# Kernel tuning notes

Hardware: AMD Instinct MI355X
Metric: run time of the kernel (lower is better)

Reference implementation:

```python
import jax, jax.numpy as jnp
import numpy as np

NUM_CLASSES = 100
EPS = 1e-07


def setup_inputs() -> dict:
    key = jax.random.key(0)
    k1, k2 = jax.random.split(key)
    N = 1_000_000
    logits = jax.random.normal(k1, (N, NUM_CLASSES), dtype=jnp.float32)
    labels = jax.random.randint(k2, (N,), 0, NUM_CLASSES, dtype=jnp.int32)
    return {"logits": logits, "labels": labels}


def reference(logits, labels):
    # pred: [N] argmax class per sample
    pred = jnp.argmax(logits, axis=1)
    C = NUM_CLASSES
    zeros = jnp.zeros((C,), dtype=jnp.float32)
    # single-pass confusion-matrix marginals (replaces per-class python loop)
    pred_count = zeros.at[pred].add(1.0)          # tp_c + fp_c
    true_count = zeros.at[labels].add(1.0)        # tp_c + fn_c
    correct = (pred == labels).astype(jnp.float32)
    tp = zeros.at[labels].add(correct)            # tp_c
    fp = pred_count - tp
    fn = true_count - tp
    precision = tp / (tp + fp + EPS)
    recall = tp / (tp + fn + EPS)
    # beta = 1 -> (1 + 1) * p * r / (1 * p + r + eps)
    f1 = 2.0 * precision * recall / (precision + recall + EPS)
    return jnp.mean(f1)
```

## Files before the change

### kernel.cpp

```cpp
#include <hip/hip_runtime.h>

#define NCLS 100
#define EPS 1e-7f

__global__ void zero_counts_kernel(unsigned int* __restrict__ counts) {
    int i = threadIdx.x;
    if (i < 3 * NCLS) counts[i] = 0u;
}

__global__ __launch_bounds__(256) void hist_kernel(
        const float* __restrict__ logits,
        const int* __restrict__ labels,
        unsigned int* __restrict__ counts,
        int N) {
    __shared__ unsigned int s_pred[NCLS];
    __shared__ unsigned int s_true[NCLS];
    __shared__ unsigned int s_tp[NCLS];
    for (int i = threadIdx.x; i < NCLS; i += blockDim.x) {
        s_pred[i] = 0u; s_true[i] = 0u; s_tp[i] = 0u;
    }
    __syncthreads();

    const int tid    = blockIdx.x * blockDim.x + threadIdx.x;
    const int q      = tid & 3;
    const int quad   = tid >> 2;
    const int nquads = (gridDim.x * blockDim.x) >> 2;

    const float4* f4base = (const float4*)logits;

    for (int row = quad; row < N; row += nquads) {
        const size_t rowf4 = (size_t)row * 25;
        const size_t A     = rowf4 & ~(size_t)3;
        const int    r3    = row & 3;

        float4 v[7];
        #pragma unroll
        for (int k = 0; k < 7; ++k) v[k] = f4base[A + 4 * k + q];

        const int off = (q - r3) << 2;

        float best = -INFINITY;
        int bidx = 0;
        #pragma unroll
        for (int k = 0; k < 7; ++k) {
            const int cb = 16 * k + off;
            float4 w = v[k];
            if ((unsigned)(cb + 0) < (unsigned)NCLS && w.x > best) { best = w.x; bidx = cb;     }
            if ((unsigned)(cb + 1) < (unsigned)NCLS && w.y > best) { best = w.y; bidx = cb + 1; }
            if ((unsigned)(cb + 2) < (unsigned)NCLS && w.z > best) { best = w.z; bidx = cb + 2; }
            if ((unsigned)(cb + 3) < (unsigned)NCLS && w.w > best) { best = w.w; bidx = cb + 3; }
        }

        #pragma unroll
        for (int m = 1; m <= 2; m <<= 1) {
            float ob = __shfl_xor(best, m, 64);
            int   oi = __shfl_xor(bidx, m, 64);
            if (ob > best || (ob == best && oi < bidx)) { best = ob; bidx = oi; }
        }

        if (q == 0) {
            int lab = labels[row];
            atomicAdd(&s_pred[bidx], 1u);
            atomicAdd(&s_true[lab], 1u);
            if (bidx == lab) atomicAdd(&s_tp[lab], 1u);
        }
    }

    __syncthreads();
    for (int i = threadIdx.x; i < NCLS; i += blockDim.x) {
        unsigned int v;
        if ((v = s_pred[i]) != 0u) atomicAdd(&counts[i], v);
        if ((v = s_true[i]) != 0u) atomicAdd(&counts[NCLS + i], v);
        if ((v = s_tp[i])   != 0u) atomicAdd(&counts[2 * NCLS + i], v);
    }
}

__global__ void finalize_kernel(const unsigned int* __restrict__ counts,
                                float* __restrict__ out) {
    __shared__ float s_f1[NCLS];
    int c = threadIdx.x;
    if (c < NCLS) {
        float tp    = (float)counts[2 * NCLS + c];
        float predc = (float)counts[c];
        float truec = (float)counts[NCLS + c];
        float fp = predc - tp;
        float fn = truec - tp;
        float precision = tp / (tp + fp + EPS);
        float recall    = tp / (tp + fn + EPS);
        float f1 = 2.0f * precision * recall / (precision + recall + EPS);
        s_f1[c] = f1;
    }
    __syncthreads();
    if (c == 0) {
        float sum = 0.0f;
        for (int i = 0; i < NCLS; ++i) sum += s_f1[i];
        out[0] = sum / (float)NCLS;
    }
}

extern "C" void kernel_launch(void* const* d_in, const int* in_sizes, int n_in,
                              void* d_out, int out_size, void* d_ws, size_t ws_size,
                              hipStream_t stream) {
    const float* logits = (const float*)d_in[0];
    const int*   labels = (const int*)d_in[1];
    float* out = (float*)d_out;
    unsigned int* counts = (unsigned int*)d_ws;

    const int N = in_sizes[1];

    zero_counts_kernel<<<1, 320, 0, stream>>>(counts);

    const int block = 256;
    const int grid  = 2048;
    hist_kernel<<<grid, block, 0, stream>>>(logits, labels, counts, N);

    finalize_kernel<<<1, 128, 0, stream>>>(counts, out);
}
```

Measured before the change: 533.0 us.

## Assign contiguous row chunks per block and double-buffer row loads

Replaces the grid-stride loop over 2048 blocks with one block per contiguous 512-row chunk, launching about 1954 blocks. Each wave now register double-buffers its row loads, issuing the next row's float4 and label loads before running argmax on the current row. The intent is to hide memory latency and improve locality for this bandwidth-bound 400MB scan. The cost is more registers per thread and a per-block shared-histogram flush that now covers fewer rows.

```diff
diff --git a/kernel.cpp b/kernel.cpp
--- a/kernel.cpp
+++ b/kernel.cpp
@@ -2,10 +2,57 @@
 
 #define NCLS 100
 #define EPS 1e-7f
+#define ROWS_PER_BLOCK 512
+#define N_ITER (ROWS_PER_BLOCK / 64)
 
 __global__ void zero_counts_kernel(unsigned int* __restrict__ counts) {
     int i = threadIdx.x;
     if (i < 3 * NCLS) counts[i] = 0u;
+}
+
+__device__ __forceinline__ void load7(const float4* __restrict__ f4,
+                                      int r, int q, int rowEnd,
+                                      float4 v[7], int* lab,
+                                      const int* __restrict__ labels) {
+    if (r < rowEnd) {
+        const size_t A = ((size_t)r * 25) & ~(size_t)3;
+        #pragma unroll
+        for (int k = 0; k < 7; ++k) v[k] = f4[A + 4 * k + q];
+        if (q == 0) *lab = labels[r];
+    }
+}
+
+__device__ __forceinline__ void process7(const float4 v[7], int r, int q,
+                                         int rowEnd, int lab,
+                                         unsigned int* s_pred,
+                                         unsigned int* s_true,
+                                         unsigned int* s_tp) {
+    float best = -INFINITY;
+    int bidx = 0;
+    if (r < rowEnd) {
+        const int r3 = r & 3;
+        const int off = (q - r3) << 2;
+        #pragma unroll
+        for (int k = 0; k < 7; ++k) {
+            const int cb = 16 * k + off;
+            float4 w = v[k];
+            if ((unsigned)(cb + 0) < (unsigned)NCLS && w.x > best) { best = w.x; bidx = cb;     }
+            if ((unsigned)(cb + 1) < (unsigned)NCLS && w.y > best) { best = w.y; bidx = cb + 1; }
+            if ((unsigned)(cb + 2) < (unsigned)NCLS && w.z > best) { best = w.z; bidx = cb + 2; }
+            if ((unsigned)(cb + 3) < (unsigned)NCLS && w.w > best) { best = w.w; bidx = cb + 3; }
+        }
+    }
+    #pragma unroll
+    for (int m = 1; m <= 2; m <<= 1) {
+        float ob = __shfl_xor(best, m, 64);
+        int   oi = __shfl_xor(bidx, m, 64);
+        if (ob > best || (ob == best && oi < bidx)) { best = ob; bidx = oi; }
+    }
+    if (q == 0 && r < rowEnd) {
+        atomicAdd(&s_pred[bidx], 1u);
+        atomicAdd(&s_true[lab], 1u);
+        if (bidx == lab) atomicAdd(&s_tp[lab], 1u);
+    }
 }
 
 __global__ __launch_bounds__(256) void hist_kernel(
@@ -21,49 +68,36 @@
     }
     __syncthreads();
 
-    const int tid    = blockIdx.x * blockDim.x + threadIdx.x;
-    const int q      = tid & 3;
-    const int quad   = tid >> 2;
-    const int nquads = (gridDim.x * blockDim.x) >> 2;
+    const int lane = threadIdx.x & 63;
+    const int wv   = threadIdx.x >> 6;
+    const int q    = lane & 3;
+    const int g    = lane >> 2;
 
-    const float4* f4base = (const float4*)logits;
+    const int blockStart = blockIdx.x * ROWS_PER_BLOCK;
+    const int rowEnd     = min(blockStart + ROWS_PER_BLOCK, N);
 
-    for (int row = quad; row < N; row += nquads) {
-        const size_t rowf4 = (size_t)row * 25;
-        const size_t A     = rowf4 & ~(size_t)3;
-        const int    r3    = row & 3;
+    const float4* f4 = (const float4*)logits;
 
-        float4 v[7];
-        #pragma unroll
-        for (int k = 0; k < 7; ++k) v[k] = f4base[A + 4 * k + q];
+    int row = blockStart + wv * 16 + g;
 
-        const int off = (q - r3) << 2;
+    float4 va[7], vb[7];
+    int la = 0, lb = 0;
 
-        float best = -INFINITY;
-        int bidx = 0;
-        #pragma unroll
-        for (int k = 0; k < 7; ++k) {
-            const int cb = 16 * k + off;
-            float4 w = v[k];
-            if ((unsigned)(cb + 0) < (unsigned)NCLS && w.x > best) { best = w.x; bidx = cb;     }
-            if ((unsigned)(cb + 1) < (unsigned)NCLS && w.y > best) { best = w.y; bidx = cb + 1; }
-            if ((unsigned)(cb + 2) < (unsigned)NCLS && w.z > best) { best = w.z; bidx = cb + 2; }
-            if ((unsigned)(cb + 3) < (unsigned)NCLS && w.w > best) { best = w.w; bidx = cb + 3; }
+    load7(f4, row, q, rowEnd, va, &la, labels);
+
+    #pragma unroll 1
+    for (int i = 0; i < N_ITER; i += 2) {
+        const int r1 = row + 64;
+        load7(f4, r1, q, rowEnd, vb, &lb, labels);
+        process7(va, row, q, rowEnd, la, s_pred, s_true, s_tp);
+
+        const int r2 = r1 + 64;
+        if (i + 2 < N_ITER) {
+            load7(f4, r2, q, rowEnd, va, &la, labels);
         }
+        process7(vb, r1, q, rowEnd, lb, s_pred, s_true, s_tp);
 
-        #pragma unroll
-        for (int m = 1; m <= 2; m <<= 1) {
-            float ob = __shfl_xor(best, m, 64);
-            int   oi = __shfl_xor(bidx, m, 64);
-            if (ob > best || (ob == best && oi < bidx)) { best = ob; bidx = oi; }
-        }
-
-        if (q == 0) {
-            int lab = labels[row];
-            atomicAdd(&s_pred[bidx], 1u);
-            atomicAdd(&s_true[lab], 1u);
-            if (bidx == lab) atomicAdd(&s_tp[lab], 1u);
-        }
+        row = r2;
     }
 
     __syncthreads();
@@ -111,7 +145,7 @@
     zero_counts_kernel<<<1, 320, 0, stream>>>(counts);
 
     const int block = 256;
-    const int grid  = 2048;
+    const int grid  = (N + ROWS_PER_BLOCK - 1) / ROWS_PER_BLOCK;
     hist_kernel<<<grid, block, 0, stream>>>(logits, labels, counts, N);
 
     finalize_kernel<<<1, 128, 0, stream>>>(counts, out);
```

Result: no change. 526.8 us (-1.2%).
